# Kernel tuning notes

Measured on AMD Instinct MI355X. Metric: run time of the kernel, lower is better.

The kernel has to match this reference:

```python
import jax, jax.numpy as jnp
import numpy as np

NUM_HEADS = 12

def setup_inputs() -> dict:
    key = jax.random.key(0)
    ks = jax.random.split(key, 6)
    B, N, C = 4, 2048, 768
    s = 0.02
    return {
        "x": jax.random.normal(ks[0], (B, N, C), jnp.float32),
        "y": jax.random.normal(ks[1], (B, N, C), jnp.float32),
        "Wq": jax.random.normal(ks[2], (C, C), jnp.float32) * s,
        "Wkv": jax.random.normal(ks[3], (2 * C, C), jnp.float32) * s,
        "tau_param": jnp.asarray(1.0, jnp.float32),
        "Wproj": jax.random.normal(ks[4], (C, C), jnp.float32) * s,
        "bproj": jnp.zeros((C,), jnp.float32),
    }

def reference(x, y, Wq, Wkv, tau_param, Wproj, bproj):
    B, N, C = x.shape
    H = NUM_HEADS
    D = C // H
    scale = D ** -0.5
    # q: [B,H,N,D]
    q = (x @ Wq.T).reshape(B, N, H, D).transpose(0, 2, 1, 3) * scale
    kv = (y @ Wkv.T).reshape(B, N, 2, H, D).transpose(2, 0, 3, 1, 4)
    k, v = kv[0], kv[1]
    tau = jax.nn.softplus(tau_param) + 1e-6
    attn = jnp.einsum("bhnd,bhmd->bhnm", q, k) / tau  # [B,H,N,N]
    attn = jax.nn.softmax(attn, axis=-1)
    out = jnp.einsum("bhnm,bhmd->bhnd", attn, v)  # [B,H,N,D]
    out = out.transpose(0, 2, 1, 3).reshape(B, N, C)
    return out @ Wproj.T + bproj
```

## Files before the change

### kernel.cpp

```cpp
#include <hip/hip_runtime.h>
#include <math.h>

typedef unsigned short u16;
typedef unsigned int u32;
typedef __fp16 fp16x2 __attribute__((ext_vector_type(2)));
typedef _Float16 half8 __attribute__((ext_vector_type(8)));
typedef float f32x4 __attribute__((ext_vector_type(4)));

#define NH   12
#define SEQ  2048
#define CDIM 768

__device__ __forceinline__ u16 f2h(float f) {
  _Float16 h = (_Float16)f;
  return __builtin_bit_cast(u16, h);
}
__device__ __forceinline__ u32 pk2(float a, float b) {
  fp16x2 h = __builtin_amdgcn_cvt_pkrtz(a, b);
  return __builtin_bit_cast(u32, h);
}
__device__ __forceinline__ void dma16(const u16* g, u16* l) {
  __builtin_amdgcn_global_load_lds(
      (const __attribute__((address_space(1))) u32*)g,
      (__attribute__((address_space(3))) u32*)l, 16, 0, 0);
}

__global__ __launch_bounds__(256) void cvt_f32_f16(const float* __restrict__ in,
                                                   u16* __restrict__ out, int n) {
  int i = (blockIdx.x * 256 + threadIdx.x) * 4;
  if (i < n) {
    float4 f = *(const float4*)(in + i);
    *(uint2*)(out + i) = make_uint2(pk2(f.x, f.y), pk2(f.z, f.w));
  }
}
__global__ __launch_bounds__(256) void cvt_f32_f16_scale(const float* __restrict__ in,
                                                         u16* __restrict__ out,
                                                         const float* __restrict__ taup, int n) {
  float t = *taup;
  float sp = (t > 20.f) ? t : log1pf(expf(t));
  float s = (0.125f / (sp + 1e-6f)) * 1.44269504088896340736f;
  int i = (blockIdx.x * 256 + threadIdx.x) * 4;
  if (i < n) {
    float4 f = *(const float4*)(in + i);
    *(uint2*)(out + i) = make_uint2(pk2(f.x * s, f.y * s), pk2(f.z * s, f.w * s));
  }
}

template<int MODE>
__global__ __launch_bounds__(128, 3) void gemm_nt(
    const u16* __restrict__ A, const u16* __restrict__ B,
    u16* __restrict__ out0, u16* __restrict__ out1,
    float* __restrict__ outf, const float* __restrict__ bias,
    int M, int N, int K)
{
  __shared__ __align__(16) u16 As[2][64 * 64];
  __shared__ __align__(16) u16 Bs[2][128 * 64];
  const int tid = threadIdx.x;
  const int wave = tid >> 6, lane = tid & 63;
  const int quad = lane >> 4, l16 = lane & 15;
  const int row0 = blockIdx.x * 64, col0 = blockIdx.y * 128;

  const int sub = lane >> 3;
  const int csw = ((lane & 7) ^ sub) * 8;

  f32x4 acc[4][4] = {};

  auto stage = [&](int k0, int bsel) {
    u16* Asp = As[bsel];
    u16* Bsp = Bs[bsel];
    #pragma unroll
    for (int i = 0; i < 4; i++) {
      int ii = wave * 4 + i;
      dma16(A + (size_t)(row0 + ii * 8 + sub) * K + k0 + csw, Asp + ii * 512);
    }
    #pragma unroll
    for (int i = 0; i < 8; i++) {
      int ii = wave * 8 + i;
      dma16(B + (size_t)(col0 + ii * 8 + sub) * K + k0 + csw, Bsp + ii * 512);
    }
  };

  stage(0, 0);
  __syncthreads();

  const int nk = K >> 6;
  for (int t = 0; t < nk; t++) {
    const int cur = t & 1;
    if (t + 1 < nk) stage((t + 1) << 6, cur ^ 1);
    const u16* Asp = As[cur];
    const u16* Bsp = Bs[cur];
    #pragma unroll
    for (int ks = 0; ks < 2; ks++) {
      half8 af[4], bfr[4];
      #pragma unroll
      for (int mt = 0; mt < 4; mt++)
        af[mt] = *(const half8*)&Asp[(mt * 16 + l16) * 64 + (((ks * 4 + quad) ^ (l16 & 7)) * 8)];
      #pragma unroll
      for (int nt = 0; nt < 4; nt++)
        bfr[nt] = *(const half8*)&Bsp[(wave * 64 + nt * 16 + l16) * 64 + (((ks * 4 + quad) ^ (l16 & 7)) * 8)];
      #pragma unroll
      for (int mt = 0; mt < 4; mt++)
        #pragma unroll
        for (int nt = 0; nt < 4; nt++)
          acc[mt][nt] = __builtin_amdgcn_mfma_f32_16x16x32_f16(af[mt], bfr[nt], acc[mt][nt], 0, 0, 0);
    }
    __syncthreads();
  }

  #pragma unroll
  for (int mt = 0; mt < 4; mt++)
  #pragma unroll
  for (int nt = 0; nt < 4; nt++)
  #pragma unroll
  for (int r = 0; r < 4; r++) {
    int gm = row0 + mt * 16 + quad * 4 + r;
    int gn = col0 + wave * 64 + nt * 16 + l16;
    float v = acc[mt][nt][r];
    if (MODE == 0) {
      int b = gm >> 11, n = gm & 2047;
      int h = gn >> 6, d = gn & 63;
      out0[(((size_t)(b * NH + h)) * SEQ + n) * 64 + d] = f2h(v);
    } else if (MODE == 1) {
      int b = gm >> 11, n = gm & 2047;
      if (gn < CDIM) {
        int h = gn >> 6, d = gn & 63;
        out0[(((size_t)(b * NH + h)) * SEQ + n) * 64 + d] = f2h(v);
      } else {
        int c = gn - CDIM;
        int h = c >> 6, d = c & 63;
        out1[(((size_t)(b * NH + h)) * 64 + d) * SEQ + n] = f2h(v);
      }
    } else {
      outf[(size_t)gm * N + gn] = v + bias[gn];
    }
  }
}

__global__ __launch_bounds__(256, 3) void attn_kernel(
    const u16* __restrict__ Q, const u16* __restrict__ Kb,
    const u16* __restrict__ Vtg, u16* __restrict__ Ob)
{
  constexpr int LDP = 72;
  __shared__ __align__(16) u16 Ks[2][64 * 64];
  __shared__ __align__(16) u16 Vs[2][64 * 64];
  __shared__ __align__(16) u16 Ps[4 * 16 * LDP];

  const int qt = blockIdx.x & 15;
  const int bh = blockIdx.x >> 4;
  const int b = bh / NH, h = bh % NH;
  const u16* Qp = Q   + (size_t)bh * SEQ * 64;
  const u16* Kp = Kb  + (size_t)bh * SEQ * 64;
  const u16* Vp = Vtg + (size_t)bh * 64 * SEQ;

  const int tid = threadIdx.x;
  const int wave = tid >> 6, lane = tid & 63;
  const int quad = lane >> 4, l16 = lane & 15;
  const int sub = lane >> 3;
  const int csw = ((lane & 7) ^ sub) * 8;
  u16* Pw = Ps + wave * 16 * LDP;

  half8 qf[2][2];
  #pragma unroll
  for (int mt = 0; mt < 2; mt++)
    #pragma unroll
    for (int ks = 0; ks < 2; ks++)
      qf[mt][ks] = *(const half8*)(Qp + (size_t)(qt * 128 + wave * 32 + mt * 16 + l16) * 64 + ks * 32 + quad * 8);

  f32x4 oacc[2][4] = {};
  float lrow[2] = {0.f, 0.f};

  auto stage = [&](int kt, int bsel) {
    #pragma unroll
    for (int i = 0; i < 2; i++) {
      int ii = wave * 2 + i;
      dma16(Kp + (size_t)(kt * 64 + ii * 8 + sub) * 64 + csw, &Ks[bsel][ii * 512]);
      dma16(Vp + (size_t)(ii * 8 + sub) * SEQ + kt * 64 + csw, &Vs[bsel][ii * 512]);
    }
  };

  stage(0, 0);
  __syncthreads();

  for (int kt = 0; kt < SEQ / 64; kt++) {
    const int cur = kt & 1;
    if (kt + 1 < SEQ / 64) stage(kt + 1, cur ^ 1);
    const u16* Ksp = Ks[cur];
    const u16* Vsp = Vs[cur];

    f32x4 sacc[2][4] = {};
    #pragma unroll
    for (int ks = 0; ks < 2; ks++) {
      #pragma unroll
      for (int ntk = 0; ntk < 4; ntk++) {
        half8 kf = *(const half8*)&Ksp[(ntk * 16 + l16) * 64 + (((ks * 4 + quad) ^ (l16 & 7)) * 8)];
        #pragma unroll
        for (int mt = 0; mt < 2; mt++)
          sacc[mt][ntk] = __builtin_amdgcn_mfma_f32_16x16x32_f16(kf, qf[mt][ks], sacc[mt][ntk], 0, 0, 0);
      }
    }

    half8 pf[2][2];
    #pragma unroll
    for (int mt = 0; mt < 2; mt++) {
      #pragma unroll
      for (int ntk = 0; ntk < 4; ntk++) {
        float p0 = exp2f(sacc[mt][ntk][0]);
        float p1 = exp2f(sacc[mt][ntk][1]);
        float p2 = exp2f(sacc[mt][ntk][2]);
        float p3 = exp2f(sacc[mt][ntk][3]);
        lrow[mt] += (p0 + p1) + (p2 + p3);
        *(uint2*)(&Pw[l16 * LDP + ntk * 16 + quad * 4]) = make_uint2(pk2(p0, p1), pk2(p2, p3));
      }
      pf[mt][0] = *(const half8*)&Pw[l16 * LDP + quad * 8];
      pf[mt][1] = *(const half8*)&Pw[l16 * LDP + 32 + quad * 8];
    }

    #pragma unroll
    for (int ks = 0; ks < 2; ks++)
      #pragma unroll
      for (int dt = 0; dt < 4; dt++) {
        half8 vf = *(const half8*)&Vsp[(dt * 16 + l16) * 64 + (((ks * 4 + quad) ^ (l16 & 7)) * 8)];
        #pragma unroll
        for (int mt = 0; mt < 2; mt++)
          oacc[mt][dt] = __builtin_amdgcn_mfma_f32_16x16x32_f16(pf[mt][ks], vf, oacc[mt][dt], 0, 0, 0);
      }

    __syncthreads();
  }

  #pragma unroll
  for (int mt = 0; mt < 2; mt++) {
    lrow[mt] += __shfl_xor(lrow[mt], 16);
    lrow[mt] += __shfl_xor(lrow[mt], 32);
  }

  #pragma unroll
  for (int mt = 0; mt < 2; mt++) {
    float lv[4];
    #pragma unroll
    for (int r = 0; r < 4; r++) lv[r] = __shfl(lrow[mt], quad * 4 + r);
    #pragma unroll
    for (int r = 0; r < 4; r++) {
      float inv = 1.0f / lv[r];
      int n = qt * 128 + wave * 32 + mt * 16 + quad * 4 + r;
      size_t base = ((size_t)b * SEQ + n) * CDIM + h * 64;
      #pragma unroll
      for (int dt = 0; dt < 4; dt++)
        Ob[base + dt * 16 + l16] = f2h(oacc[mt][dt][r] * inv);
    }
  }
}

extern "C" void kernel_launch(void* const* d_in, const int* in_sizes, int n_in,
                              void* d_out, int out_size, void* d_ws, size_t ws_size,
                              hipStream_t stream)
{
  const float* x     = (const float*)d_in[0];
  const float* y     = (const float*)d_in[1];
  const float* Wq    = (const float*)d_in[2];
  const float* Wkv   = (const float*)d_in[3];
  const float* taup  = (const float*)d_in[4];
  const float* Wproj = (const float*)d_in[5];
  const float* bproj = (const float*)d_in[6];
  float* out = (float*)d_out;

  char* ws = (char*)d_ws;
  size_t off = 0;
  auto alloc = [&](size_t bytes) { char* p = ws + off; off += bytes; return p; };
  u16* xh  = (u16*)alloc(8192ull * 768 * 2);
  u16* yh  = (u16*)alloc(8192ull * 768 * 2);
  u16* wqh = (u16*)alloc(768ull * 768 * 2);
  u16* wkh = (u16*)alloc(1536ull * 768 * 2);
  u16* wph = (u16*)alloc(768ull * 768 * 2);
  u16* qb  = (u16*)alloc(8192ull * 768 * 2);
  u16* kb  = (u16*)alloc(8192ull * 768 * 2);
  u16* vtb = (u16*)alloc(8192ull * 768 * 2);
  u16* ao  = (u16*)alloc(8192ull * 768 * 2);

  cvt_f32_f16<<<6144, 256, 0, stream>>>(x, xh, 8192 * 768);
  cvt_f32_f16<<<6144, 256, 0, stream>>>(y, yh, 8192 * 768);
  cvt_f32_f16_scale<<<576, 256, 0, stream>>>(Wq, wqh, taup, 768 * 768);
  cvt_f32_f16<<<1152, 256, 0, stream>>>(Wkv, wkh, 1536 * 768);
  cvt_f32_f16<<<576, 256, 0, stream>>>(Wproj, wph, 768 * 768);

  gemm_nt<0><<<dim3(128, 6), 128, 0, stream>>>(xh, wqh, qb, nullptr, nullptr, nullptr, 8192, 768, 768);
  gemm_nt<1><<<dim3(128, 12), 128, 0, stream>>>(yh, wkh, kb, vtb, nullptr, nullptr, 8192, 1536, 768);
  attn_kernel<<<dim3(48 * 16), 256, 0, stream>>>(qb, kb, vtb, ao);
  gemm_nt<2><<<dim3(128, 6), 128, 0, stream>>>(ao, wph, nullptr, nullptr, out, bproj, 8192, 768, 768);
}
```

Baseline: 272.8 us.

## Enlarge GEMM tiles, remap attention blocks, and compute softmax row sums via MFMA

The GEMM moves to 128x128 tiles with four waves in a 2x2 layout, which raises operand reuse per block and halves the block count. In attention, a block-index swizzle spreads heads across XCDs, and s_setprio is raised around the MFMA phases. The softmax denominator is now accumulated by an extra MFMA against a ones vector instead of scalar adds and shuffles. exp2f is also replaced with the hardware exp2 builtin. These changes cut VALU and shuffle work, at the cost of more LDS per GEMM block and a few extra MFMAs per tile.

```diff
diff --git a/kernel.cpp b/kernel.cpp
--- a/kernel.cpp
+++ b/kernel.cpp
@@ -47,18 +47,19 @@
 }
 
 template<int MODE>
-__global__ __launch_bounds__(128, 3) void gemm_nt(
+__global__ __launch_bounds__(256, 2) void gemm_nt(
     const u16* __restrict__ A, const u16* __restrict__ B,
     u16* __restrict__ out0, u16* __restrict__ out1,
     float* __restrict__ outf, const float* __restrict__ bias,
     int M, int N, int K)
 {
-  __shared__ __align__(16) u16 As[2][64 * 64];
+  __shared__ __align__(16) u16 As[2][128 * 64];
   __shared__ __align__(16) u16 Bs[2][128 * 64];
   const int tid = threadIdx.x;
   const int wave = tid >> 6, lane = tid & 63;
   const int quad = lane >> 4, l16 = lane & 15;
-  const int row0 = blockIdx.x * 64, col0 = blockIdx.y * 128;
+  const int wr = wave >> 1, wc = wave & 1;
+  const int row0 = blockIdx.x * 128, col0 = blockIdx.y * 128;
 
   const int sub = lane >> 3;
   const int csw = ((lane & 7) ^ sub) * 8;
@@ -72,10 +73,6 @@
     for (int i = 0; i < 4; i++) {
       int ii = wave * 4 + i;
       dma16(A + (size_t)(row0 + ii * 8 + sub) * K + k0 + csw, Asp + ii * 512);
-    }
-    #pragma unroll
-    for (int i = 0; i < 8; i++) {
-      int ii = wave * 8 + i;
       dma16(B + (size_t)(col0 + ii * 8 + sub) * K + k0 + csw, Bsp + ii * 512);
     }
   };
@@ -94,10 +91,10 @@
       half8 af[4], bfr[4];
       #pragma unroll
       for (int mt = 0; mt < 4; mt++)
-        af[mt] = *(const half8*)&Asp[(mt * 16 + l16) * 64 + (((ks * 4 + quad) ^ (l16 & 7)) * 8)];
+        af[mt] = *(const half8*)&Asp[(wr * 64 + mt * 16 + l16) * 64 + (((ks * 4 + quad) ^ (l16 & 7)) * 8)];
       #pragma unroll
       for (int nt = 0; nt < 4; nt++)
-        bfr[nt] = *(const half8*)&Bsp[(wave * 64 + nt * 16 + l16) * 64 + (((ks * 4 + quad) ^ (l16 & 7)) * 8)];
+        bfr[nt] = *(const half8*)&Bsp[(wc * 64 + nt * 16 + l16) * 64 + (((ks * 4 + quad) ^ (l16 & 7)) * 8)];
       #pragma unroll
       for (int mt = 0; mt < 4; mt++)
         #pragma unroll
@@ -113,8 +110,8 @@
   for (int nt = 0; nt < 4; nt++)
   #pragma unroll
   for (int r = 0; r < 4; r++) {
-    int gm = row0 + mt * 16 + quad * 4 + r;
-    int gn = col0 + wave * 64 + nt * 16 + l16;
+    int gm = row0 + wr * 64 + mt * 16 + quad * 4 + r;
+    int gn = col0 + wc * 64 + nt * 16 + l16;
     float v = acc[mt][nt][r];
     if (MODE == 0) {
       int b = gm >> 11, n = gm & 2047;
@@ -145,8 +142,9 @@
   __shared__ __align__(16) u16 Vs[2][64 * 64];
   __shared__ __align__(16) u16 Ps[4 * 16 * LDP];
 
-  const int qt = blockIdx.x & 15;
-  const int bh = blockIdx.x >> 4;
+  const int bid = (blockIdx.x & 7) * 96 + (blockIdx.x >> 3);
+  const int qt = bid & 15;
+  const int bh = bid >> 4;
   const int b = bh / NH, h = bh % NH;
   const u16* Qp = Q   + (size_t)bh * SEQ * 64;
   const u16* Kp = Kb  + (size_t)bh * SEQ * 64;
@@ -159,6 +157,10 @@
   const int csw = ((lane & 7) ^ sub) * 8;
   u16* Pw = Ps + wave * 16 * LDP;
 
+  half8 vone;
+  #pragma unroll
+  for (int j = 0; j < 8; j++) vone[j] = (_Float16)1.0f;
+
   half8 qf[2][2];
   #pragma unroll
   for (int mt = 0; mt < 2; mt++)
@@ -167,7 +169,7 @@
       qf[mt][ks] = *(const half8*)(Qp + (size_t)(qt * 128 + wave * 32 + mt * 16 + l16) * 64 + ks * 32 + quad * 8);
 
   f32x4 oacc[2][4] = {};
-  float lrow[2] = {0.f, 0.f};
+  f32x4 lacc[2] = {};
 
   auto stage = [&](int kt, int bsel) {
     #pragma unroll
@@ -188,6 +190,7 @@
     const u16* Vsp = Vs[cur];
 
     f32x4 sacc[2][4] = {};
+    __builtin_amdgcn_s_setprio(1);
     #pragma unroll
     for (int ks = 0; ks < 2; ks++) {
       #pragma unroll
@@ -198,25 +201,26 @@
           sacc[mt][ntk] = __builtin_amdgcn_mfma_f32_16x16x32_f16(kf, qf[mt][ks], sacc[mt][ntk], 0, 0, 0);
       }
     }
+    __builtin_amdgcn_s_setprio(0);
 
     half8 pf[2][2];
     #pragma unroll
     for (int mt = 0; mt < 2; mt++) {
       #pragma unroll
       for (int ntk = 0; ntk < 4; ntk++) {
-        float p0 = exp2f(sacc[mt][ntk][0]);
-        float p1 = exp2f(sacc[mt][ntk][1]);
-        float p2 = exp2f(sacc[mt][ntk][2]);
-        float p3 = exp2f(sacc[mt][ntk][3]);
-        lrow[mt] += (p0 + p1) + (p2 + p3);
+        float p0 = __builtin_amdgcn_exp2f(sacc[mt][ntk][0]);
+        float p1 = __builtin_amdgcn_exp2f(sacc[mt][ntk][1]);
+        float p2 = __builtin_amdgcn_exp2f(sacc[mt][ntk][2]);
+        float p3 = __builtin_amdgcn_exp2f(sacc[mt][ntk][3]);
         *(uint2*)(&Pw[l16 * LDP + ntk * 16 + quad * 4]) = make_uint2(pk2(p0, p1), pk2(p2, p3));
       }
       pf[mt][0] = *(const half8*)&Pw[l16 * LDP + quad * 8];
       pf[mt][1] = *(const half8*)&Pw[l16 * LDP + 32 + quad * 8];
     }
 
-    #pragma unroll
-    for (int ks = 0; ks < 2; ks++)
+    __builtin_amdgcn_s_setprio(1);
+    #pragma unroll
+    for (int ks = 0; ks < 2; ks++) {
       #pragma unroll
       for (int dt = 0; dt < 4; dt++) {
         half8 vf = *(const half8*)&Vsp[(dt * 16 + l16) * 64 + (((ks * 4 + quad) ^ (l16 & 7)) * 8)];
@@ -224,24 +228,20 @@
         for (int mt = 0; mt < 2; mt++)
           oacc[mt][dt] = __builtin_amdgcn_mfma_f32_16x16x32_f16(pf[mt][ks], vf, oacc[mt][dt], 0, 0, 0);
       }
+      #pragma unroll
+      for (int mt = 0; mt < 2; mt++)
+        lacc[mt] = __builtin_amdgcn_mfma_f32_16x16x32_f16(pf[mt][ks], vone, lacc[mt], 0, 0, 0);
+    }
+    __builtin_amdgcn_s_setprio(0);
 
     __syncthreads();
   }
 
   #pragma unroll
   for (int mt = 0; mt < 2; mt++) {
-    lrow[mt] += __shfl_xor(lrow[mt], 16);
-    lrow[mt] += __shfl_xor(lrow[mt], 32);
-  }
-
-  #pragma unroll
-  for (int mt = 0; mt < 2; mt++) {
-    float lv[4];
-    #pragma unroll
-    for (int r = 0; r < 4; r++) lv[r] = __shfl(lrow[mt], quad * 4 + r);
     #pragma unroll
     for (int r = 0; r < 4; r++) {
-      float inv = 1.0f / lv[r];
+      float inv = 1.0f / lacc[mt][r];
       int n = qt * 128 + wave * 32 + mt * 16 + quad * 4 + r;
       size_t base = ((size_t)b * SEQ + n) * CDIM + h * 64;
       #pragma unroll
@@ -283,8 +283,8 @@
   cvt_f32_f16<<<1152, 256, 0, stream>>>(Wkv, wkh, 1536 * 768);
   cvt_f32_f16<<<576, 256, 0, stream>>>(Wproj, wph, 768 * 768);
 
-  gemm_nt<0><<<dim3(128, 6), 128, 0, stream>>>(xh, wqh, qb, nullptr, nullptr, nullptr, 8192, 768, 768);
-  gemm_nt<1><<<dim3(128, 12), 128, 0, stream>>>(yh, wkh, kb, vtb, nullptr, nullptr, 8192, 1536, 768);
+  gemm_nt<0><<<dim3(64, 6), 256, 0, stream>>>(xh, wqh, qb, nullptr, nullptr, nullptr, 8192, 768, 768);
+  gemm_nt<1><<<dim3(64, 12), 256, 0, stream>>>(yh, wkh, kb, vtb, nullptr, nullptr, 8192, 1536, 768);
   attn_kernel<<<dim3(48 * 16), 256, 0, stream>>>(qb, kb, vtb, ao);
-  gemm_nt<2><<<dim3(128, 6), 128, 0, stream>>>(ao, wph, nullptr, nullptr, out, bproj, 8192, 768, 768);
-}
+  gemm_nt<2><<<dim3(64, 6), 256, 0, stream>>>(ao, wph, nullptr, nullptr, out, bproj, 8192, 768, 768);
+}
```

Measured after the change: 250.9 us. 8.0% less time.
